# Kernel tuning notes

Hardware: AMD Instinct MI355X
Metric: run time of the kernel (lower is better)

## Reference

```python
import jax, jax.numpy as jnp
import numpy as np

N0, N1, N2 = 262144, 65536, 16384   # sampled src nodes, layer-1 targets, layer-2 targets
E1, E2 = 1048576, 262144            # fanout 16 edges per layer
IN_C, HID_C, OUT_C = 128, 256, 64


def sage_conv(x_src, x_dst, src, dst, num_dst, W_l, W_r, b):
    # PyG SAGEConv (mean aggr): out = mean_{j in N(i)} x_src[j] @ W_l^T + b + x_dst @ W_r^T
    msgs = x_src[src]                                   # [E, C] gather
    s = jax.ops.segment_sum(msgs, dst, num_segments=num_dst)
    cnt = jax.ops.segment_sum(jnp.ones((src.shape[0],), x_src.dtype), dst,
                              num_segments=num_dst)
    aggr = s / jnp.maximum(cnt, 1.0)[:, None]           # mean; isolated nodes -> 0
    return aggr @ W_l.T + b + x_dst @ W_r.T


def setup_inputs() -> dict:
    key = jax.random.key(0)
    ks = jax.random.split(key, 9)
    inp = {
        "x": jax.random.normal(ks[0], (N0, IN_C), dtype=jnp.float32),
        "src1": jax.random.randint(ks[1], (E1,), 0, N0, dtype=jnp.int32),
        "dst1": jax.random.randint(ks[2], (E1,), 0, N1, dtype=jnp.int32),
        "src2": jax.random.randint(ks[3], (E2,), 0, N1, dtype=jnp.int32),
        "dst2": jax.random.randint(ks[4], (E2,), 0, N2, dtype=jnp.int32),
        "W1_l": jax.random.normal(ks[5], (HID_C, IN_C), dtype=jnp.float32) * 0.05,
        "W1_r": jax.random.normal(ks[6], (HID_C, IN_C), dtype=jnp.float32) * 0.05,
        "b1": jnp.zeros((HID_C,), dtype=jnp.float32),
        "W2_l": jax.random.normal(ks[7], (OUT_C, HID_C), dtype=jnp.float32) * 0.05,
        "W2_r": jax.random.normal(ks[8], (OUT_C, HID_C), dtype=jnp.float32) * 0.05,
        "b2": jnp.zeros((OUT_C,), dtype=jnp.float32),
    }
    return inp


def reference(x, src1, dst1, src2, dst2, W1_l, W1_r, b1, W2_l, W2_r, b2):
    # layer 1: sources = all N0 nodes, targets = first N1 nodes (x_target = x[:size[1]])
    h = sage_conv(x, x[:N1], src1, dst1, N1, W1_l, W1_r, b1)   # [N1, HID_C]
    h = jax.nn.relu(h)   # dropout is identity in eval mode
    # layer 2: sources = N1 layer-1 outputs, targets = first N2
    h = sage_conv(h, h[:N2], src2, dst2, N2, W2_l, W2_r, b2)   # [N2, OUT_C]
    return jax.nn.log_softmax(h, axis=-1)
```

## Files before the change

### kernel.cpp

```cpp
#include <hip/hip_runtime.h>
#include <cstdint>
#include <cstddef>

#define N0C 262144
#define N1C 65536
#define N2C 16384
#define E1C 1048576
#define E2C 262144

typedef __attribute__((ext_vector_type(8))) short bf16x8;
typedef __attribute__((ext_vector_type(4))) float f32x4;

__device__ __forceinline__ unsigned short f2bf(float f) {
  union { float f; unsigned u; } q; q.f = f;
  unsigned r = q.u + 0x7fffu + ((q.u >> 16) & 1u);
  return (unsigned short)(r >> 16);
}
__device__ __forceinline__ float blo(unsigned u) {
  union { unsigned u; float f; } q; q.u = u << 16; return q.f;
}
__device__ __forceinline__ float bhi(unsigned u) {
  union { unsigned u; float f; } q; q.u = u & 0xffff0000u; return q.f;
}
__device__ __forceinline__ void gl_lds16(const void* g, void* l) {
  __builtin_amdgcn_global_load_lds((const __attribute__((address_space(1))) void*)g,
                                   (__attribute__((address_space(3))) void*)l, 16, 0, 0);
}

__global__ __launch_bounds__(256) void cvtw_kernel(
    const float4* __restrict__ W1l, const float4* __restrict__ W1r,
    const float4* __restrict__ W2l, const float4* __restrict__ W2r,
    ushort4* __restrict__ W1lb, ushort4* __restrict__ W1rb,
    ushort4* __restrict__ W2lb, ushort4* __restrict__ W2rb,
    int* __restrict__ btail) {
  int y = blockIdx.y;
  int i = blockIdx.x * 256 + threadIdx.x;
  if (y == 4) {
    if (i < 512) btail[i] = 0;
    return;
  }
  const float4* in; ushort4* outp; int n4;
  if (y == 0)      { in = W1l; outp = W1lb; n4 = 8192; }
  else if (y == 1) { in = W1r; outp = W1rb; n4 = 8192; }
  else if (y == 2) { in = W2l; outp = W2lb; n4 = 4096; }
  else             { in = W2r; outp = W2rb; n4 = 4096; }
  if (i < n4) {
    float4 v = in[i];
    ushort4 o;
    o.x = f2bf(v.x); o.y = f2bf(v.y); o.z = f2bf(v.z); o.w = f2bf(v.w);
    outp[i] = o;
  }
}

__global__ __launch_bounds__(256) void mega_kernel(
    const int* __restrict__ src1, const int* __restrict__ dst1,
    const int* __restrict__ src2, const int* __restrict__ dst2,
    int* __restrict__ btail, unsigned* __restrict__ pair1, unsigned* __restrict__ pair2,
    const float4* __restrict__ x, ushort4* __restrict__ xb) {
  __shared__ int hist[256];
  __shared__ int lofs[256];
  __shared__ int gbase[256];
  __shared__ unsigned stg[4096];
  __shared__ unsigned char bstg[4096];
  int b = blockIdx.x;
  int t = threadIdx.x;
  if (b >= 320) {
    int i = (b - 320) * 256 + t;
    const int stride = 2048 * 256;
    const int n4 = N0C * 128 / 4;
    for (; i < n4; i += stride) {
      float4 v = x[i];
      ushort4 o;
      o.x = f2bf(v.x); o.y = f2bf(v.y); o.z = f2bf(v.z); o.w = f2bf(v.w);
      xb[i] = o;
    }
    return;
  }
  const int* src; const int* dst; int shift; int dmask; int* bt; unsigned* pb; int e0;
  if (b < 256) { src = src1; dst = dst1; shift = 8; dmask = 255; bt = btail;       pb = pair1; e0 = b * 4096; }
  else         { src = src2; dst = dst2; shift = 6; dmask = 63;  bt = btail + 256; pb = pair2; e0 = (b - 256) * 4096; }
  hist[t] = 0;
  __syncthreads();
  unsigned pk[16]; int bk[16], rk[16];
#pragma unroll
  for (int k = 0; k < 16; ++k) {
    int e = e0 + k * 256 + t;
    int s = src[e];
    int d = dst[e];
    bk[k] = d >> shift;
    pk[k] = ((unsigned)(d & dmask) << 18) | (unsigned)s;
    rk[k] = atomicAdd(&hist[bk[k]], 1);
  }
  __syncthreads();
  int v = hist[t];
  lofs[t] = v;
  __syncthreads();
  for (int ofs = 1; ofs < 256; ofs <<= 1) {
    int add = (t >= ofs) ? lofs[t - ofs] : 0;
    __syncthreads();
    lofs[t] += add;
    __syncthreads();
  }
  gbase[t] = atomicAdd(&bt[t], v);
  int excl = lofs[t] - v;
  lofs[t] = excl;
  __syncthreads();
#pragma unroll
  for (int k = 0; k < 16; ++k) {
    int p = lofs[bk[k]] + rk[k];
    stg[p] = pk[k];
    bstg[p] = (unsigned char)bk[k];
  }
  __syncthreads();
  for (int i = t; i < 4096; i += 256) {
    int bki = bstg[i];
    int idx = gbase[bki] + (i - lofs[bki]);
    if (idx < 8192)
      pb[(size_t)bki * 8192 + idx] = stg[i];
  }
}

__global__ __launch_bounds__(256) void binB_kernel(
    const unsigned* __restrict__ pair1, const unsigned* __restrict__ pair2,
    const int* __restrict__ btail,
    int* __restrict__ off1, int* __restrict__ cnt1, int* __restrict__ ssrc1,
    int* __restrict__ off2, int* __restrict__ cnt2, int* __restrict__ ssrc2) {
  __shared__ int lcnt[256];
  __shared__ int loff[256];
  __shared__ int lcnt2[256];
  __shared__ unsigned stage[8192];
  int b = blockIdx.x;
  int t = threadIdx.x;
  const unsigned* pb; const int* bt; int dpb; int* off; int* cnt; int* ssrc; int bl;
  if (b < 256) { bl = b;       pb = pair1 + (size_t)bl * 8192; bt = btail;       dpb = 256; off = off1; cnt = cnt1; ssrc = ssrc1; }
  else         { bl = b - 256; pb = pair2 + (size_t)bl * 8192; bt = btail + 256; dpb = 64;  off = off2; cnt = cnt2; ssrc = ssrc2; }
  lcnt[t] = (t < bl) ? bt[t] : 0;
  __syncthreads();
  for (int ofs = 128; ofs > 0; ofs >>= 1) {
    if (t < ofs) lcnt[t] += lcnt[t + ofs];
    __syncthreads();
  }
  int base = lcnt[0];
  __syncthreads();
  lcnt[t] = 0;
  lcnt2[t] = 0;
  __syncthreads();
  int n = bt[bl];
  if (n > 8192) n = 8192;
  for (int i = t; i < n; i += 256) {
    unsigned p = pb[i];
    atomicAdd(&lcnt[p >> 18], 1);
  }
  __syncthreads();
  int v = lcnt[t];
  loff[t] = v;
  __syncthreads();
  for (int ofs = 1; ofs < 256; ofs <<= 1) {
    int add = (t >= ofs) ? loff[t - ofs] : 0;
    __syncthreads();
    loff[t] += add;
    __syncthreads();
  }
  int excl = loff[t] - v;
  loff[t] = excl;
  if (t < dpb) {
    cnt[bl * dpb + t] = v;
    off[bl * dpb + t] = base + excl;
  }
  __syncthreads();
  for (int i = t; i < n; i += 256) {
    unsigned p = pb[i];
    int dl = p >> 18;
    int r = atomicAdd(&lcnt2[dl], 1);
    stage[loff[dl] + r] = p & 0x3FFFFu;
  }
  __syncthreads();
  for (int i = t; i < n; i += 256) ssrc[base + i] = (int)stage[i];
}

__global__ __launch_bounds__(256) void agg1_kernel(const ushort* __restrict__ xb,
                                                   const int* __restrict__ ssrc,
                                                   const int* __restrict__ off,
                                                   const int* __restrict__ cnt,
                                                   ushort* __restrict__ aggr) {
  int wid = (blockIdx.x * 256 + threadIdx.x) >> 6;
  int lane = threadIdx.x & 63;
  int grp = lane >> 4;
  int cl = lane & 15;
  int start = __builtin_amdgcn_readfirstlane(off[wid]);
  int n = __builtin_amdgcn_readfirstlane(cnt[wid]);
  float a0 = 0.f, a1 = 0.f, a2 = 0.f, a3 = 0.f, a4 = 0.f, a5 = 0.f, a6 = 0.f, a7 = 0.f;
  int j = 0;
  for (; j + 8 <= n; j += 8) {
    int sa = ssrc[start + j + grp];
    int sb = ssrc[start + j + 4 + grp];
    uint4 va = *(const uint4*)(xb + (size_t)sa * 128 + cl * 8);
    uint4 vb = *(const uint4*)(xb + (size_t)sb * 128 + cl * 8);
    a0 += blo(va.x) + blo(vb.x); a1 += bhi(va.x) + bhi(vb.x);
    a2 += blo(va.y) + blo(vb.y); a3 += bhi(va.y) + bhi(vb.y);
    a4 += blo(va.z) + blo(vb.z); a5 += bhi(va.z) + bhi(vb.z);
    a6 += blo(va.w) + blo(vb.w); a7 += bhi(va.w) + bhi(vb.w);
  }
  if (j + 4 <= n) {
    int s = ssrc[start + j + grp];
    uint4 v = *(const uint4*)(xb + (size_t)s * 128 + cl * 8);
    a0 += blo(v.x); a1 += bhi(v.x); a2 += blo(v.y); a3 += bhi(v.y);
    a4 += blo(v.z); a5 += bhi(v.z); a6 += blo(v.w); a7 += bhi(v.w);
    j += 4;
  }
  if (grp < n - j) {
    int s = ssrc[start + j + grp];
    uint4 v = *(const uint4*)(xb + (size_t)s * 128 + cl * 8);
    a0 += blo(v.x); a1 += bhi(v.x); a2 += blo(v.y); a3 += bhi(v.y);
    a4 += blo(v.z); a5 += bhi(v.z); a6 += blo(v.w); a7 += bhi(v.w);
  }
#define RED1(v) v += __shfl_xor(v, 16); v += __shfl_xor(v, 32);
  RED1(a0) RED1(a1) RED1(a2) RED1(a3) RED1(a4) RED1(a5) RED1(a6) RED1(a7)
#undef RED1
  if (lane < 16) {
    float inv = (n > 0) ? 1.0f / (float)n : 0.f;
    uint4 o;
    o.x = (unsigned)f2bf(a0 * inv) | ((unsigned)f2bf(a1 * inv) << 16);
    o.y = (unsigned)f2bf(a2 * inv) | ((unsigned)f2bf(a3 * inv) << 16);
    o.z = (unsigned)f2bf(a4 * inv) | ((unsigned)f2bf(a5 * inv) << 16);
    o.w = (unsigned)f2bf(a6 * inv) | ((unsigned)f2bf(a7 * inv) << 16);
    *(uint4*)(aggr + (size_t)wid * 128 + cl * 8) = o;
  }
}

__global__ __launch_bounds__(256) void agg2_kernel(const ushort* __restrict__ h1b,
                                                   const int* __restrict__ ssrc,
                                                   const int* __restrict__ off,
                                                   const int* __restrict__ cnt,
                                                   ushort* __restrict__ aggr) {
  int wid = (blockIdx.x * 256 + threadIdx.x) >> 6;
  int lane = threadIdx.x & 63;
  int grp = lane >> 5;
  int cl = lane & 31;
  int start = __builtin_amdgcn_readfirstlane(off[wid]);
  int n = __builtin_amdgcn_readfirstlane(cnt[wid]);
  float a0 = 0.f, a1 = 0.f, a2 = 0.f, a3 = 0.f, a4 = 0.f, a5 = 0.f, a6 = 0.f, a7 = 0.f;
  int j = 0;
  for (; j + 8 <= n; j += 8) {
    int s0 = ssrc[start + j + grp];
    int s1 = ssrc[start + j + 2 + grp];
    int s2 = ssrc[start + j + 4 + grp];
    int s3 = ssrc[start + j + 6 + grp];
    uint4 v0 = *(const uint4*)(h1b + (size_t)s0 * 256 + cl * 8);
    uint4 v1 = *(const uint4*)(h1b + (size_t)s1 * 256 + cl * 8);
    uint4 v2 = *(const uint4*)(h1b + (size_t)s2 * 256 + cl * 8);
    uint4 v3 = *(const uint4*)(h1b + (size_t)s3 * 256 + cl * 8);
    a0 += blo(v0.x) + blo(v1.x) + blo(v2.x) + blo(v3.x);
    a1 += bhi(v0.x) + bhi(v1.x) + bhi(v2.x) + bhi(v3.x);
    a2 += blo(v0.y) + blo(v1.y) + blo(v2.y) + blo(v3.y);
    a3 += bhi(v0.y) + bhi(v1.y) + bhi(v2.y) + bhi(v3.y);
    a4 += blo(v0.z) + blo(v1.z) + blo(v2.z) + blo(v3.z);
    a5 += bhi(v0.z) + bhi(v1.z) + bhi(v2.z) + bhi(v3.z);
    a6 += blo(v0.w) + blo(v1.w) + blo(v2.w) + blo(v3.w);
    a7 += bhi(v0.w) + bhi(v1.w) + bhi(v2.w) + bhi(v3.w);
  }
  for (; j + 2 <= n; j += 2) {
    int s = ssrc[start + j + grp];
    uint4 v = *(const uint4*)(h1b + (size_t)s * 256 + cl * 8);
    a0 += blo(v.x); a1 += bhi(v.x); a2 += blo(v.y); a3 += bhi(v.y);
    a4 += blo(v.z); a5 += bhi(v.z); a6 += blo(v.w); a7 += bhi(v.w);
  }
  if (grp < n - j) {
    int s = ssrc[start + j + grp];
    uint4 v = *(const uint4*)(h1b + (size_t)s * 256 + cl * 8);
    a0 += blo(v.x); a1 += bhi(v.x); a2 += blo(v.y); a3 += bhi(v.y);
    a4 += blo(v.z); a5 += bhi(v.z); a6 += blo(v.w); a7 += bhi(v.w);
  }
#define RED2(v) v += __shfl_xor(v, 32);
  RED2(a0) RED2(a1) RED2(a2) RED2(a3) RED2(a4) RED2(a5) RED2(a6) RED2(a7)
#undef RED2
  if (lane < 32) {
    float inv = (n > 0) ? 1.0f / (float)n : 0.f;
    uint4 o;
    o.x = (unsigned)f2bf(a0 * inv) | ((unsigned)f2bf(a1 * inv) << 16);
    o.y = (unsigned)f2bf(a2 * inv) | ((unsigned)f2bf(a3 * inv) << 16);
    o.z = (unsigned)f2bf(a4 * inv) | ((unsigned)f2bf(a5 * inv) << 16);
    o.w = (unsigned)f2bf(a6 * inv) | ((unsigned)f2bf(a7 * inv) << 16);
    *(uint4*)(aggr + (size_t)wid * 256 + cl * 8) = o;
  }
}

__global__ __launch_bounds__(512) void mgemm1_kernel(
    const ushort* __restrict__ aggr1, const ushort* __restrict__ xb,
    const ushort* __restrict__ W1lb, const ushort* __restrict__ W1rb,
    const float* __restrict__ b1, ushort* __restrict__ h1b) {
  __shared__ ushort smem[24576];
  ushort* sA = smem;
  ushort* sB = smem + 8192;
  int t = threadIdx.x;
  int lane = t & 63;
  int w = t >> 6;
  int wm = w >> 2, wn = w & 3;
  int i0 = blockIdx.x * 128;

  int sr = t >> 3;
  int sc = (t & 7) ^ (sr & 7);
  int quad = lane >> 4;
  int l15 = lane & 15;
  int xorv = lane & 7;

  f32x4 acc[4][4];
#pragma unroll
  for (int i = 0; i < 4; ++i)
#pragma unroll
    for (int j = 0; j < 4; ++j) acc[i][j] = (f32x4)(0.f);

  for (int kt = 0; kt < 4; ++kt) {
    const ushort* Asrc = (kt < 2) ? aggr1 : xb;
    const ushort* Bsrc = (kt < 2) ? W1lb : W1rb;
    int koff = (kt & 1) * 64;
#pragma unroll
    for (int it = 0; it < 2; ++it) {
      int r = it * 64 + sr;
      gl_lds16(Asrc + (size_t)(i0 + r) * 128 + koff + sc * 8, sA + (it * 512 + t) * 8);
    }
#pragma unroll
    for (int it = 0; it < 4; ++it) {
      int r = it * 64 + sr;
      gl_lds16(Bsrc + (size_t)r * 128 + koff + sc * 8, sB + (it * 512 + t) * 8);
    }
    __syncthreads();
#pragma unroll
    for (int s = 0; s < 2; ++s) {
      int chunk = ((s * 4 + quad) ^ xorv) * 8;
      bf16x8 av[4], bv[4];
#pragma unroll
      for (int fi = 0; fi < 4; ++fi)
        av[fi] = *(const bf16x8*)(sA + (wm * 64 + fi * 16 + l15) * 64 + chunk);
#pragma unroll
      for (int fj = 0; fj < 4; ++fj)
        bv[fj] = *(const bf16x8*)(sB + (wn * 64 + fj * 16 + l15) * 64 + chunk);
#pragma unroll
      for (int fi = 0; fi < 4; ++fi)
#pragma unroll
        for (int fj = 0; fj < 4; ++fj)
          acc[fi][fj] = __builtin_amdgcn_mfma_f32_16x16x32_bf16(av[fi], bv[fj], acc[fi][fj], 0, 0, 0);
    }
    __syncthreads();
  }

  for (int ph = 0; ph < 2; ++ph) {
    if (wm == ph) {
      ushort* eb = smem + (w & 3) * 4096;
#pragma unroll
      for (int fj = 0; fj < 4; ++fj) {
        float bias = b1[wn * 64 + fj * 16 + l15];
#pragma unroll
        for (int fi = 0; fi < 4; ++fi)
#pragma unroll
          for (int r = 0; r < 4; ++r) {
            float v = fmaxf(acc[fi][fj][r] + bias, 0.f);
            eb[(fi * 16 + quad * 4 + r) * 64 + fj * 16 + l15] = f2bf(v);
          }
      }
#pragma unroll
      for (int i = 0; i < 16; ++i) {
        int row = i * 4 + (lane >> 4);
        uint2 v = *(const uint2*)(eb + row * 64 + l15 * 4);
        *(uint2*)(h1b + (size_t)(i0 + wm * 64 + row) * 256 + wn * 64 + l15 * 4) = v;
      }
    }
    __syncthreads();
  }
}

__global__ __launch_bounds__(256) void mgemm2_kernel(
    const ushort* __restrict__ aggr2, const ushort* __restrict__ h1b,
    const ushort* __restrict__ W2lb, const ushort* __restrict__ W2rb,
    const float* __restrict__ b2, float* __restrict__ out) {
  __shared__ ushort sA[64 * 64];
  __shared__ ushort sB[64 * 64];
  int t = threadIdx.x;
  int lane = t & 63;
  int w = t >> 6;
  int i0 = blockIdx.x * 64;

  int sr = t >> 3;
  int sc = (t & 7) ^ (sr & 7);
  int quad = lane >> 4;
  int l15 = lane & 15;
  int xorv = lane & 7;

  f32x4 acc[4];
#pragma unroll
  for (int j = 0; j < 4; ++j) acc[j] = (f32x4)(0.f);

  for (int kt = 0; kt < 8; ++kt) {
    const ushort* Asrc = (kt < 4) ? aggr2 : h1b;
    const ushort* Bsrc = (kt < 4) ? W2lb : W2rb;
    int koff = (kt & 3) * 64;
#pragma unroll
    for (int it = 0; it < 2; ++it) {
      int r = it * 32 + sr;
      gl_lds16(Asrc + (size_t)(i0 + r) * 256 + koff + sc * 8, sA + (it * 256 + t) * 8);
    }
#pragma unroll
    for (int it = 0; it < 2; ++it) {
      int r = it * 32 + sr;
      gl_lds16(Bsrc + (size_t)r * 256 + koff + sc * 8, sB + (it * 256 + t) * 8);
    }
    __syncthreads();
#pragma unroll
    for (int s = 0; s < 2; ++s) {
      int chunk = ((s * 4 + quad) ^ xorv) * 8;
      bf16x8 av = *(const bf16x8*)(sA + (w * 16 + l15) * 64 + chunk);
      bf16x8 bv[4];
#pragma unroll
      for (int fj = 0; fj < 4; ++fj)
        bv[fj] = *(const bf16x8*)(sB + (fj * 16 + l15) * 64 + chunk);
#pragma unroll
      for (int fj = 0; fj < 4; ++fj)
        acc[fj] = __builtin_amdgcn_mfma_f32_16x16x32_bf16(av, bv[fj], acc[fj], 0, 0, 0);
    }
    __syncthreads();
  }

  float b2c[4];
#pragma unroll
  for (int fj = 0; fj < 4; ++fj) b2c[fj] = b2[fj * 16 + l15];

#pragma unroll
  for (int r = 0; r < 4; ++r) {
    int row = i0 + w * 16 + quad * 4 + r;
    float v[4];
#pragma unroll
    for (int fj = 0; fj < 4; ++fj) v[fj] = acc[fj][r] + b2c[fj];
    float m = fmaxf(fmaxf(v[0], v[1]), fmaxf(v[2], v[3]));
    m = fmaxf(m, __shfl_xor(m, 1));
    m = fmaxf(m, __shfl_xor(m, 2));
    m = fmaxf(m, __shfl_xor(m, 4));
    m = fmaxf(m, __shfl_xor(m, 8));
    float ssum = __expf(v[0] - m) + __expf(v[1] - m) + __expf(v[2] - m) + __expf(v[3] - m);
    ssum += __shfl_xor(ssum, 1);
    ssum += __shfl_xor(ssum, 2);
    ssum += __shfl_xor(ssum, 4);
    ssum += __shfl_xor(ssum, 8);
    float lg = m + __logf(ssum);
#pragma unroll
    for (int fj = 0; fj < 4; ++fj)
      out[(size_t)row * 64 + fj * 16 + l15] = v[fj] - lg;
  }
}


extern "C" void kernel_launch(void* const* d_in, const int* in_sizes, int n_in,
                              void* d_out, int out_size, void* d_ws, size_t ws_size,
                              hipStream_t stream) {
  const float* x   = (const float*)d_in[0];
  const int* src1  = (const int*)d_in[1];
  const int* dst1  = (const int*)d_in[2];
  const int* src2  = (const int*)d_in[3];
  const int* dst2  = (const int*)d_in[4];
  const float* W1l = (const float*)d_in[5];
  const float* W1r = (const float*)d_in[6];
  const float* b1  = (const float*)d_in[7];
  const float* W2l = (const float*)d_in[8];
  const float* W2r = (const float*)d_in[9];
  const float* b2  = (const float*)d_in[10];
  float* out = (float*)d_out;

  char* base = (char*)d_ws;
  ushort* xb   = (ushort*)base;
  ushort* ag1b = (ushort*)(base + 67108864);
  ushort* ag2b = (ushort*)(base + 83886080);
  unsigned* pair1 = (unsigned*)(base + 92274688);
  unsigned* pair2 = (unsigned*)(base + 100663296);
  ushort* h1b  = (ushort*)(base + 109051904);
  int* cnt1  = (int*)(base + 142606336);
  int* off1  = cnt1 + N1C;
  int* cnt2  = off1 + N1C;
  int* off2  = cnt2 + N2C;
  int* btail = off2 + N2C;
  int* ssrc1 = btail + 512;
  int* ssrc2 = ssrc1 + E1C;
  ushort* W1lb = (ushort*)(ssrc2 + E2C);
  ushort* W1rb = W1lb + 32768;
  ushort* W2lb = W1rb + 32768;
  ushort* W2rb = W2lb + 16384;

  cvtw_kernel<<<dim3(32, 5), 256, 0, stream>>>(
      (const float4*)W1l, (const float4*)W1r, (const float4*)W2l, (const float4*)W2r,
      (ushort4*)W1lb, (ushort4*)W1rb, (ushort4*)W2lb, (ushort4*)W2rb, btail);

  mega_kernel<<<2368, 256, 0, stream>>>(src1, dst1, src2, dst2, btail, pair1, pair2,
                                        (const float4*)x, (ushort4*)xb);

  binB_kernel<<<512, 256, 0, stream>>>(pair1, pair2, btail,
                                       off1, cnt1, ssrc1, off2, cnt2, ssrc2);

  agg1_kernel<<<N1C / 4, 256, 0, stream>>>(xb, ssrc1, off1, cnt1, ag1b);
  mgemm1_kernel<<<N1C / 128, 512, 0, stream>>>(ag1b, xb, W1lb, W1rb, b1, h1b);

  agg2_kernel<<<N2C / 4, 256, 0, stream>>>(h1b, ssrc2, off2, cnt2, ag2b);
  mgemm2_kernel<<<N2C / 64, 256, 0, stream>>>(ag2b, h1b, W2lb, W2rb, b2, out);
}
```

Baseline: 154.1 us.

## Fuse layer-1 neighbor aggregation into the layer-1 GEMM via LDS staging

Replaces the separate agg1 kernel and mgemm1 kernel with one kernel. Each 512-thread block first gathers and mean-aggregates its 128 target rows into a swizzled LDS buffer, then runs the MFMA GEMM reading the aggregated half of the A operand straight from LDS. This removes the global write and re-read of the 16 MB bf16 aggregate and one kernel launch. In exchange, LDS per block grows to 80 KB, which lowers occupancy, and the gather phase now runs on only 512 blocks with 16 sequential rows per wave, so there may be less memory-level parallelism for the random gathers.

```diff
diff --git a/kernel.cpp b/kernel.cpp
--- a/kernel.cpp
+++ b/kernel.cpp
@@ -178,53 +178,148 @@
   for (int i = t; i < n; i += 256) ssrc[base + i] = (int)stage[i];
 }
 
-__global__ __launch_bounds__(256) void agg1_kernel(const ushort* __restrict__ xb,
-                                                   const int* __restrict__ ssrc,
-                                                   const int* __restrict__ off,
-                                                   const int* __restrict__ cnt,
-                                                   ushort* __restrict__ aggr) {
-  int wid = (blockIdx.x * 256 + threadIdx.x) >> 6;
-  int lane = threadIdx.x & 63;
-  int grp = lane >> 4;
-  int cl = lane & 15;
-  int start = __builtin_amdgcn_readfirstlane(off[wid]);
-  int n = __builtin_amdgcn_readfirstlane(cnt[wid]);
-  float a0 = 0.f, a1 = 0.f, a2 = 0.f, a3 = 0.f, a4 = 0.f, a5 = 0.f, a6 = 0.f, a7 = 0.f;
-  int j = 0;
-  for (; j + 8 <= n; j += 8) {
-    int sa = ssrc[start + j + grp];
-    int sb = ssrc[start + j + 4 + grp];
-    uint4 va = *(const uint4*)(xb + (size_t)sa * 128 + cl * 8);
-    uint4 vb = *(const uint4*)(xb + (size_t)sb * 128 + cl * 8);
-    a0 += blo(va.x) + blo(vb.x); a1 += bhi(va.x) + bhi(vb.x);
-    a2 += blo(va.y) + blo(vb.y); a3 += bhi(va.y) + bhi(vb.y);
-    a4 += blo(va.z) + blo(vb.z); a5 += bhi(va.z) + bhi(vb.z);
-    a6 += blo(va.w) + blo(vb.w); a7 += bhi(va.w) + bhi(vb.w);
-  }
-  if (j + 4 <= n) {
-    int s = ssrc[start + j + grp];
-    uint4 v = *(const uint4*)(xb + (size_t)s * 128 + cl * 8);
-    a0 += blo(v.x); a1 += bhi(v.x); a2 += blo(v.y); a3 += bhi(v.y);
-    a4 += blo(v.z); a5 += bhi(v.z); a6 += blo(v.w); a7 += bhi(v.w);
-    j += 4;
-  }
-  if (grp < n - j) {
-    int s = ssrc[start + j + grp];
-    uint4 v = *(const uint4*)(xb + (size_t)s * 128 + cl * 8);
-    a0 += blo(v.x); a1 += bhi(v.x); a2 += blo(v.y); a3 += bhi(v.y);
-    a4 += blo(v.z); a5 += bhi(v.z); a6 += blo(v.w); a7 += bhi(v.w);
-  }
-#define RED1(v) v += __shfl_xor(v, 16); v += __shfl_xor(v, 32);
-  RED1(a0) RED1(a1) RED1(a2) RED1(a3) RED1(a4) RED1(a5) RED1(a6) RED1(a7)
-#undef RED1
-  if (lane < 16) {
-    float inv = (n > 0) ? 1.0f / (float)n : 0.f;
-    uint4 o;
-    o.x = (unsigned)f2bf(a0 * inv) | ((unsigned)f2bf(a1 * inv) << 16);
-    o.y = (unsigned)f2bf(a2 * inv) | ((unsigned)f2bf(a3 * inv) << 16);
-    o.z = (unsigned)f2bf(a4 * inv) | ((unsigned)f2bf(a5 * inv) << 16);
-    o.w = (unsigned)f2bf(a6 * inv) | ((unsigned)f2bf(a7 * inv) << 16);
-    *(uint4*)(aggr + (size_t)wid * 128 + cl * 8) = o;
+__global__ __launch_bounds__(512) void fgemm1_kernel(
+    const ushort* __restrict__ xb,
+    const int* __restrict__ ssrc, const int* __restrict__ off, const int* __restrict__ cnt,
+    const ushort* __restrict__ W1lb, const ushort* __restrict__ W1rb,
+    const float* __restrict__ b1, ushort* __restrict__ h1b) {
+  __shared__ ushort smem[40960];
+  ushort* sAgg = smem;
+  ushort* sA = smem + 16384;
+  ushort* sB = smem + 24576;
+  int t = threadIdx.x;
+  int lane = t & 63;
+  int w = t >> 6;
+  int wm = w >> 2, wn = w & 3;
+  int i0 = blockIdx.x * 128;
+
+  {
+    int grp = lane >> 4;
+    int cl = lane & 15;
+    for (int rr = 0; rr < 16; ++rr) {
+      int row = w * 16 + rr;
+      int gid = i0 + row;
+      int start = __builtin_amdgcn_readfirstlane(off[gid]);
+      int n = __builtin_amdgcn_readfirstlane(cnt[gid]);
+      float a0 = 0.f, a1 = 0.f, a2 = 0.f, a3 = 0.f, a4 = 0.f, a5 = 0.f, a6 = 0.f, a7 = 0.f;
+      int j = 0;
+      for (; j + 8 <= n; j += 8) {
+        int sa = ssrc[start + j + grp];
+        int sb = ssrc[start + j + 4 + grp];
+        uint4 va = *(const uint4*)(xb + (size_t)sa * 128 + cl * 8);
+        uint4 vb = *(const uint4*)(xb + (size_t)sb * 128 + cl * 8);
+        a0 += blo(va.x) + blo(vb.x); a1 += bhi(va.x) + bhi(vb.x);
+        a2 += blo(va.y) + blo(vb.y); a3 += bhi(va.y) + bhi(vb.y);
+        a4 += blo(va.z) + blo(vb.z); a5 += bhi(va.z) + bhi(vb.z);
+        a6 += blo(va.w) + blo(vb.w); a7 += bhi(va.w) + bhi(vb.w);
+      }
+      if (j + 4 <= n) {
+        int s = ssrc[start + j + grp];
+        uint4 v = *(const uint4*)(xb + (size_t)s * 128 + cl * 8);
+        a0 += blo(v.x); a1 += bhi(v.x); a2 += blo(v.y); a3 += bhi(v.y);
+        a4 += blo(v.z); a5 += bhi(v.z); a6 += blo(v.w); a7 += bhi(v.w);
+        j += 4;
+      }
+      if (grp < n - j) {
+        int s = ssrc[start + j + grp];
+        uint4 v = *(const uint4*)(xb + (size_t)s * 128 + cl * 8);
+        a0 += blo(v.x); a1 += bhi(v.x); a2 += blo(v.y); a3 += bhi(v.y);
+        a4 += blo(v.z); a5 += bhi(v.z); a6 += blo(v.w); a7 += bhi(v.w);
+      }
+#define REDF(v) v += __shfl_xor(v, 16); v += __shfl_xor(v, 32);
+      REDF(a0) REDF(a1) REDF(a2) REDF(a3) REDF(a4) REDF(a5) REDF(a6) REDF(a7)
+#undef REDF
+      if (lane < 16) {
+        float inv = (n > 0) ? 1.0f / (float)n : 0.f;
+        uint4 o;
+        o.x = (unsigned)f2bf(a0 * inv) | ((unsigned)f2bf(a1 * inv) << 16);
+        o.y = (unsigned)f2bf(a2 * inv) | ((unsigned)f2bf(a3 * inv) << 16);
+        o.z = (unsigned)f2bf(a4 * inv) | ((unsigned)f2bf(a5 * inv) << 16);
+        o.w = (unsigned)f2bf(a6 * inv) | ((unsigned)f2bf(a7 * inv) << 16);
+        *(uint4*)(sAgg + row * 128 + (cl ^ (row & 15)) * 8) = o;
+      }
+    }
+  }
+  __syncthreads();
+
+  int sr = t >> 3;
+  int sc = (t & 7) ^ (sr & 7);
+  int quad = lane >> 4;
+  int l15 = lane & 15;
+  int xorv = lane & 7;
+
+  f32x4 acc[4][4];
+#pragma unroll
+  for (int i = 0; i < 4; ++i)
+#pragma unroll
+    for (int j = 0; j < 4; ++j) acc[i][j] = (f32x4)(0.f);
+
+  for (int kt = 0; kt < 4; ++kt) {
+    const ushort* Bsrc = (kt < 2) ? W1lb : W1rb;
+    int koff = (kt & 1) * 64;
+    if (kt >= 2) {
+#pragma unroll
+      for (int it = 0; it < 2; ++it) {
+        int r = it * 64 + sr;
+        gl_lds16(xb + (size_t)(i0 + r) * 128 + koff + sc * 8, sA + (it * 512 + t) * 8);
+      }
+    }
+#pragma unroll
+    for (int it = 0; it < 4; ++it) {
+      int r = it * 64 + sr;
+      gl_lds16(Bsrc + (size_t)r * 128 + koff + sc * 8, sB + (it * 512 + t) * 8);
+    }
+    __syncthreads();
+#pragma unroll
+    for (int s = 0; s < 2; ++s) {
+      int cbase = (s * 4 + quad) ^ xorv;
+      bf16x8 av[4], bv[4];
+      if (kt < 2) {
+        int g = kt * 8 + s * 4 + quad;
+#pragma unroll
+        for (int fi = 0; fi < 4; ++fi) {
+          int row = wm * 64 + fi * 16 + l15;
+          av[fi] = *(const bf16x8*)(sAgg + row * 128 + (g ^ (row & 15)) * 8);
+        }
+      } else {
+#pragma unroll
+        for (int fi = 0; fi < 4; ++fi)
+          av[fi] = *(const bf16x8*)(sA + (wm * 64 + fi * 16 + l15) * 64 + cbase * 8);
+      }
+#pragma unroll
+      for (int fj = 0; fj < 4; ++fj)
+        bv[fj] = *(const bf16x8*)(sB + (wn * 64 + fj * 16 + l15) * 64 + cbase * 8);
+#pragma unroll
+      for (int fi = 0; fi < 4; ++fi)
+#pragma unroll
+        for (int fj = 0; fj < 4; ++fj)
+          acc[fi][fj] = __builtin_amdgcn_mfma_f32_16x16x32_bf16(av[fi], bv[fj], acc[fi][fj], 0, 0, 0);
+    }
+    __syncthreads();
+  }
+
+  for (int ph = 0; ph < 2; ++ph) {
+    if (wm == ph) {
+      ushort* eb = smem + (w & 3) * 4096;
+#pragma unroll
+      for (int fj = 0; fj < 4; ++fj) {
+        float bias = b1[wn * 64 + fj * 16 + l15];
+#pragma unroll
+        for (int fi = 0; fi < 4; ++fi)
+#pragma unroll
+          for (int r = 0; r < 4; ++r) {
+            float v = fmaxf(acc[fi][fj][r] + bias, 0.f);
+            eb[(fi * 16 + quad * 4 + r) * 64 + fj * 16 + l15] = f2bf(v);
+          }
+      }
+#pragma unroll
+      for (int i = 0; i < 16; ++i) {
+        int row = i * 4 + (lane >> 4);
+        uint2 v = *(const uint2*)(eb + row * 64 + l15 * 4);
+        *(uint2*)(h1b + (size_t)(i0 + wm * 64 + row) * 256 + wn * 64 + l15 * 4) = v;
+      }
+    }
+    __syncthreads();
   }
 }
 
@@ -285,90 +380,6 @@
   }
 }
 
-__global__ __launch_bounds__(512) void mgemm1_kernel(
-    const ushort* __restrict__ aggr1, const ushort* __restrict__ xb,
-    const ushort* __restrict__ W1lb, const ushort* __restrict__ W1rb,
-    const float* __restrict__ b1, ushort* __restrict__ h1b) {
-  __shared__ ushort smem[24576];
-  ushort* sA = smem;
-  ushort* sB = smem + 8192;
-  int t = threadIdx.x;
-  int lane = t & 63;
-  int w = t >> 6;
-  int wm = w >> 2, wn = w & 3;
-  int i0 = blockIdx.x * 128;
-
-  int sr = t >> 3;
-  int sc = (t & 7) ^ (sr & 7);
-  int quad = lane >> 4;
-  int l15 = lane & 15;
-  int xorv = lane & 7;
-
-  f32x4 acc[4][4];
-#pragma unroll
-  for (int i = 0; i < 4; ++i)
-#pragma unroll
-    for (int j = 0; j < 4; ++j) acc[i][j] = (f32x4)(0.f);
-
-  for (int kt = 0; kt < 4; ++kt) {
-    const ushort* Asrc = (kt < 2) ? aggr1 : xb;
-    const ushort* Bsrc = (kt < 2) ? W1lb : W1rb;
-    int koff = (kt & 1) * 64;
-#pragma unroll
-    for (int it = 0; it < 2; ++it) {
-      int r = it * 64 + sr;
-      gl_lds16(Asrc + (size_t)(i0 + r) * 128 + koff + sc * 8, sA + (it * 512 + t) * 8);
-    }
-#pragma unroll
-    for (int it = 0; it < 4; ++it) {
-      int r = it * 64 + sr;
-      gl_lds16(Bsrc + (size_t)r * 128 + koff + sc * 8, sB + (it * 512 + t) * 8);
-    }
-    __syncthreads();
-#pragma unroll
-    for (int s = 0; s < 2; ++s) {
-      int chunk = ((s * 4 + quad) ^ xorv) * 8;
-      bf16x8 av[4], bv[4];
-#pragma unroll
-      for (int fi = 0; fi < 4; ++fi)
-        av[fi] = *(const bf16x8*)(sA + (wm * 64 + fi * 16 + l15) * 64 + chunk);
-#pragma unroll
-      for (int fj = 0; fj < 4; ++fj)
-        bv[fj] = *(const bf16x8*)(sB + (wn * 64 + fj * 16 + l15) * 64 + chunk);
-#pragma unroll
-      for (int fi = 0; fi < 4; ++fi)
-#pragma unroll
-        for (int fj = 0; fj < 4; ++fj)
-          acc[fi][fj] = __builtin_amdgcn_mfma_f32_16x16x32_bf16(av[fi], bv[fj], acc[fi][fj], 0, 0, 0);
-    }
-    __syncthreads();
-  }
-
-  for (int ph = 0; ph < 2; ++ph) {
-    if (wm == ph) {
-      ushort* eb = smem + (w & 3) * 4096;
-#pragma unroll
-      for (int fj = 0; fj < 4; ++fj) {
-        float bias = b1[wn * 64 + fj * 16 + l15];
-#pragma unroll
-        for (int fi = 0; fi < 4; ++fi)
-#pragma unroll
-          for (int r = 0; r < 4; ++r) {
-            float v = fmaxf(acc[fi][fj][r] + bias, 0.f);
-            eb[(fi * 16 + quad * 4 + r) * 64 + fj * 16 + l15] = f2bf(v);
-          }
-      }
-#pragma unroll
-      for (int i = 0; i < 16; ++i) {
-        int row = i * 4 + (lane >> 4);
-        uint2 v = *(const uint2*)(eb + row * 64 + l15 * 4);
-        *(uint2*)(h1b + (size_t)(i0 + wm * 64 + row) * 256 + wn * 64 + l15 * 4) = v;
-      }
-    }
-    __syncthreads();
-  }
-}
-
 __global__ __launch_bounds__(256) void mgemm2_kernel(
     const ushort* __restrict__ aggr2, const ushort* __restrict__ h1b,
     const ushort* __restrict__ W2lb, const ushort* __restrict__ W2rb,
@@ -466,12 +477,11 @@
 
   char* base = (char*)d_ws;
   ushort* xb   = (ushort*)base;
-  ushort* ag1b = (ushort*)(base + 67108864);
-  ushort* ag2b = (ushort*)(base + 83886080);
-  unsigned* pair1 = (unsigned*)(base + 92274688);
-  unsigned* pair2 = (unsigned*)(base + 100663296);
-  ushort* h1b  = (ushort*)(base + 109051904);
-  int* cnt1  = (int*)(base + 142606336);
+  ushort* ag2b = (ushort*)(base + 67108864);
+  unsigned* pair1 = (unsigned*)(base + 75497472);
+  unsigned* pair2 = (unsigned*)(base + 83886080);
+  ushort* h1b  = (ushort*)(base + 92274688);
+  int* cnt1  = (int*)(base + 125829120);
   int* off1  = cnt1 + N1C;
   int* cnt2  = off1 + N1C;
   int* off2  = cnt2 + N2C;
@@ -493,8 +503,8 @@
   binB_kernel<<<512, 256, 0, stream>>>(pair1, pair2, btail,
                                        off1, cnt1, ssrc1, off2, cnt2, ssrc2);
 
-  agg1_kernel<<<N1C / 4, 256, 0, stream>>>(xb, ssrc1, off1, cnt1, ag1b);
-  mgemm1_kernel<<<N1C / 128, 512, 0, stream>>>(ag1b, xb, W1lb, W1rb, b1, h1b);
+  fgemm1_kernel<<<N1C / 128, 512, 0, stream>>>(xb, ssrc1, off1, cnt1,
+                                               W1lb, W1rb, b1, h1b);
 
   agg2_kernel<<<N2C / 4, 256, 0, stream>>>(h1b, ssrc2, off2, cnt2, ag2b);
   mgemm2_kernel<<<N2C / 64, 256, 0, stream>>>(ag2b, h1b, W2lb, W2rb, b2, out);
```

New measurement: 189.1 us. +22.7%, slower.
